# Optimization experiments

Hardware: AMD Instinct MI355X
Metric: run time of the kernel (lower is better)

Reference implementation:

```python
import jax, jax.numpy as jnp
import numpy as np

NEG_SLOPE = 0.2
EPS = 1e-16  # matches PyG softmax epsilon


def gat_conv(x, src, dst, W, att_src, att_dst, bias):
    """PyG-style GATConv (concat heads, self-loops already in src/dst).
    x: [N, F_in]; W: [F_in, H*C]; att_*: [H, C]; bias: [H*C]."""
    N = x.shape[0]
    H, C = att_src.shape
    h = (x @ W).reshape(N, H, C)                       # [N,H,C]
    a_src = jnp.einsum('nhc,hc->nh', h, att_src)       # [N,H]
    a_dst = jnp.einsum('nhc,hc->nh', h, att_dst)
    e = jax.nn.leaky_relu(a_src[src] + a_dst[dst], NEG_SLOPE)   # [E,H]
    # segment softmax over incoming edges of each dst node
    e_max = jax.ops.segment_max(e, dst, num_segments=N)         # [N,H]
    e_max = jnp.where(jnp.isfinite(e_max), e_max, 0.0)
    e_exp = jnp.exp(e - e_max[dst])                              # [E,H]
    denom = jax.ops.segment_sum(e_exp, dst, num_segments=N)     # [N,H]
    alpha = e_exp / (denom[dst] + EPS)                           # [E,H]
    msg = h[src] * alpha[:, :, None]                             # [E,H,C]
    out = jax.ops.segment_sum(msg, dst, num_segments=N)         # [N,H,C]
    return out.reshape(N, H * C) + bias


def setup_inputs() -> dict:
    key = jax.random.key(0)
    ks = jax.random.split(key, 16)
    N, E = 50000, 800000
    F_in, C, H = 1280, 32, 8
    HC = H * C
    NG = 64  # graphs in batch
    x = jax.random.normal(ks[0], (N, F_in), dtype=jnp.float32)
    edge_index = jax.random.randint(ks[1], (2, E), 0, N, dtype=jnp.int64)
    batch = jnp.sort(jax.random.randint(ks[2], (N,), 0, NG, dtype=jnp.int64))
    s = 1.0 / np.sqrt(F_in)
    W1 = jax.random.normal(ks[3], (F_in, HC), dtype=jnp.float32) * s
    as1 = jax.random.normal(ks[4], (H, C), dtype=jnp.float32) * 0.1
    ad1 = jax.random.normal(ks[5], (H, C), dtype=jnp.float32) * 0.1
    b1 = jnp.zeros((HC,), dtype=jnp.float32)
    s2 = 1.0 / np.sqrt(HC)
    W2 = jax.random.normal(ks[6], (HC, HC), dtype=jnp.float32) * s2
    as2 = jax.random.normal(ks[7], (H, C), dtype=jnp.float32) * 0.1
    ad2 = jax.random.normal(ks[8], (H, C), dtype=jnp.float32) * 0.1
    b2 = jnp.zeros((HC,), dtype=jnp.float32)
    lin1_w = jax.random.normal(ks[9], (HC, 128), dtype=jnp.float32) * s2
    lin1_b = jnp.zeros((128,), dtype=jnp.float32)
    lin2_w = jax.random.normal(ks[10], (128, 1), dtype=jnp.float32) * (1.0 / np.sqrt(128))
    lin2_b = jnp.zeros((1,), dtype=jnp.float32)
    return {"x": x, "edge_index": edge_index, "batch": batch,
            "W1": W1, "as1": as1, "ad1": ad1, "b1": b1,
            "W2": W2, "as2": as2, "ad2": ad2, "b2": b2,
            "lin1_w": lin1_w, "lin1_b": lin1_b, "lin2_w": lin2_w, "lin2_b": lin2_b}


def reference(x, edge_index, batch, W1, as1, ad1, b1, W2, as2, ad2, b2,
              lin1_w, lin1_b, lin2_w, lin2_b):
    N = x.shape[0]
    NG = 64
    loops = jnp.arange(N, dtype=edge_index.dtype)
    src = jnp.concatenate([edge_index[0], loops])  # add self-loops (PyG default)
    dst = jnp.concatenate([edge_index[1], loops])
    h = jax.nn.relu(gat_conv(x, src, dst, W1, as1, ad1, b1))
    h = jax.nn.relu(gat_conv(h, src, dst, W2, as2, ad2, b2))
    # global mean pool over graphs
    sums = jax.ops.segment_sum(h, batch, num_segments=NG)               # [NG,HC]
    cnts = jax.ops.segment_sum(jnp.ones((N, 1), h.dtype), batch, num_segments=NG)
    pooled = sums / jnp.maximum(cnts, 1.0)
    z = jax.nn.relu(pooled @ lin1_w + lin1_b)
    out = z @ lin2_w + lin2_b                                            # [NG,1]
    return out.squeeze(-1)
```

## Files before the change

### kernel.cpp

```cpp
#include <hip/hip_runtime.h>
#include <hip/hip_bf16.h>
#include <math.h>

#define HC 256
#define NH 8
#define NEG_SLOPE 0.2f
#define CHW 64

typedef unsigned short u16;
typedef __attribute__((ext_vector_type(8))) short bf16x8;
typedef __attribute__((ext_vector_type(4))) short bf16x4;
typedef __attribute__((ext_vector_type(4))) float f32x4;

__device__ __forceinline__ u16 f2bf(float f) {
    unsigned int u = __float_as_uint(f);
    u += 0x7FFFu + ((u >> 16) & 1u);
    return (u16)(u >> 16);
}
__device__ __forceinline__ float bf2f(u16 s) {
    return __uint_as_float(((unsigned int)s) << 16);
}
__device__ __forceinline__ f32x4 bf4f(ushort4 v) {
    f32x4 r;
    r[0] = bf2f(v.x); r[1] = bf2f(v.y); r[2] = bf2f(v.z); r[3] = bf2f(v.w);
    return r;
}

__global__ __launch_bounds__(256) void pack_b_split(const float* __restrict__ B, int K,
                                                    u16* __restrict__ Bh,
                                                    u16* __restrict__ Bl) {
    const int g = blockIdx.x * 256 + threadIdx.x;
    const int lane = g & 63;
    const int f = (g >> 6) & 15;
    const int kt = g >> 10;
    const int col = f * 16 + (lane & 15);
    const int k0 = kt * 32 + (lane >> 4) * 8;
    bf16x8 hv, lv;
#pragma unroll
    for (int e = 0; e < 8; e++) {
        const float v = B[(size_t)(k0 + e) * HC + col];
        const u16 h = f2bf(v);
        hv[e] = (short)h;
        lv[e] = (short)f2bf(v - bf2f(h));
    }
    const size_t off = (size_t)g * 8;
    *(bf16x8*)(Bh + off) = hv;
    *(bf16x8*)(Bl + off) = lv;
}

__global__ __launch_bounds__(256) void gemm_fused_split(
    const float* __restrict__ A,
    const u16* __restrict__ Bh, const u16* __restrict__ Bl,
    float* __restrict__ C, int M, int K) {
    __shared__ u16 ldsA[2][2048];
    const int tid = threadIdx.x;
    const int wid = tid >> 6;
    const int lane = tid & 63;
    const int rowblk = blockIdx.x;
    const int KT = K >> 5;

    f32x4 acc[4][4];
#pragma unroll
    for (int i = 0; i < 4; i++)
#pragma unroll
        for (int j = 0; j < 4; j++) acc[i][j] = (f32x4)0.f;

    const int srow = wid * 16 + (lane & 15);
    const int skq = (lane >> 4) * 8;
    const int grow = rowblk * 64 + srow;
    const float* aptr = (grow < M) ? (A + (size_t)grow * K + skq) : nullptr;
    const int wslot = wid * 512 + lane * 8;

    auto cvt_store = [&](int buf, float4 v0, float4 v1) {
        const float vv[8] = {v0.x, v0.y, v0.z, v0.w, v1.x, v1.y, v1.z, v1.w};
        bf16x8 hv;
#pragma unroll
        for (int e = 0; e < 8; e++) hv[e] = (short)f2bf(vv[e]);
        *(bf16x8*)&ldsA[buf][wslot] = hv;
    };

    float4 p0 = make_float4(0.f, 0.f, 0.f, 0.f), p1 = p0;
    if (aptr) {
        p0 = *(const float4*)(aptr);
        p1 = *(const float4*)(aptr + 4);
    }
    cvt_store(0, p0, p1);
    p0 = make_float4(0.f, 0.f, 0.f, 0.f); p1 = p0;
    if (aptr && KT > 1) {
        p0 = *(const float4*)(aptr + 32);
        p1 = *(const float4*)(aptr + 36);
    }
    __syncthreads();

    int cur = 0;
    for (int kt = 0; kt < KT; kt++) {
        const u16* bHp = Bh + ((size_t)kt * 16 + wid * 4) * 512 + lane * 8;
        const u16* bLp = Bl + ((size_t)kt * 16 + wid * 4) * 512 + lane * 8;
        bf16x8 bh[4], bl[4];
#pragma unroll
        for (int j = 0; j < 4; j++) {
            bh[j] = *(const bf16x8*)(bHp + j * 512);
            bl[j] = *(const bf16x8*)(bLp + j * 512);
        }
        const u16* base = &ldsA[cur][lane * 8];
        bf16x8 ah[4];
#pragma unroll
        for (int i = 0; i < 4; i++) ah[i] = *(const bf16x8*)(base + i * 512);

        if (kt + 1 < KT) {
            cvt_store(cur ^ 1, p0, p1);
            p0 = make_float4(0.f, 0.f, 0.f, 0.f); p1 = p0;
            if (aptr && kt + 2 < KT) {
                p0 = *(const float4*)(aptr + (kt + 2) * 32);
                p1 = *(const float4*)(aptr + (kt + 2) * 32 + 4);
            }
        }
#pragma unroll
        for (int i = 0; i < 4; i++)
#pragma unroll
            for (int j = 0; j < 4; j++) {
                acc[i][j] = __builtin_amdgcn_mfma_f32_16x16x32_bf16(ah[i], bh[j], acc[i][j], 0, 0, 0);
                acc[i][j] = __builtin_amdgcn_mfma_f32_16x16x32_bf16(ah[i], bl[j], acc[i][j], 0, 0, 0);
            }
        __syncthreads();
        cur ^= 1;
    }

    const int r0 = rowblk * 64;
    const int colb = wid * 64 + (lane & 15);
#pragma unroll
    for (int i = 0; i < 4; i++) {
#pragma unroll
        for (int r = 0; r < 4; r++) {
            const int row = r0 + i * 16 + (lane >> 4) * 4 + r;
            if (row < M) {
#pragma unroll
                for (int j = 0; j < 4; j++)
                    C[(size_t)row * HC + colb + j * 16] = acc[i][j][r];
            }
        }
    }
}

__global__ __launch_bounds__(256) void attn_coef(const float* __restrict__ h,
                                                 const float* __restrict__ att_s,
                                                 const float* __restrict__ att_d,
                                                 float* __restrict__ a_src,
                                                 float* __restrict__ a_dst,
                                                 u16* __restrict__ h_bf) {
    const int n = blockIdx.x;
    const int tid = threadIdx.x;
    const float hv = h[(size_t)n * HC + tid];
    h_bf[(size_t)n * HC + tid] = f2bf(hv);
    float p = hv * att_s[tid];
    float q = hv * att_d[tid];
#pragma unroll
    for (int m = 16; m >= 1; m >>= 1) {
        p += __shfl_xor(p, m);
        q += __shfl_xor(q, m);
    }
    if ((tid & 31) == 0) {
        a_src[n * NH + (tid >> 5)] = p;
        a_dst[n * NH + (tid >> 5)] = q;
    }
}

__global__ void count_deg(const int* __restrict__ dst, int E, int ET, int* __restrict__ deg) {
    const int e = blockIdx.x * blockDim.x + threadIdx.x;
    if (e >= ET) return;
    const int d = (e < E) ? dst[e] : (e - E);
    atomicAdd(&deg[d], 1);
}

__global__ __launch_bounds__(256) void scan_block(const int* __restrict__ deg,
                                                  int* __restrict__ row_ptr,
                                                  int* __restrict__ partials, int N) {
    __shared__ int sd[256];
    const int tid = threadIdx.x;
    const int base = blockIdx.x * 1024 + tid * 4;
    int v0 = (base + 0 < N) ? deg[base + 0] : 0;
    int v1 = (base + 1 < N) ? deg[base + 1] : 0;
    int v2 = (base + 2 < N) ? deg[base + 2] : 0;
    int v3 = (base + 3 < N) ? deg[base + 3] : 0;
    const int tsum = v0 + v1 + v2 + v3;
    sd[tid] = tsum;
    __syncthreads();
    int run = tsum;
    for (int off = 1; off < 256; off <<= 1) {
        int t = 0;
        if (tid >= off) t = sd[tid - off];
        __syncthreads();
        run += t;
        sd[tid] = run;
        __syncthreads();
    }
    const int excl = run - tsum;
    int s0 = excl + v0, s1 = s0 + v1, s2 = s1 + v2, s3 = s2 + v3;
    if (base + 0 < N) row_ptr[base + 1] = s0;
    if (base + 1 < N) row_ptr[base + 2] = s1;
    if (base + 2 < N) row_ptr[base + 3] = s2;
    if (base + 3 < N) row_ptr[base + 4] = s3;
    if (tid == 255) partials[blockIdx.x] = run;
}

__global__ __launch_bounds__(1024) void scan_partials(int* __restrict__ partials, int nb) {
    __shared__ int sd[1024];
    const int tid = threadIdx.x;
    int v = (tid < nb) ? partials[tid] : 0;
    sd[tid] = v;
    __syncthreads();
    int run = v;
    for (int off = 1; off < 1024; off <<= 1) {
        int t = 0;
        if (tid >= off) t = sd[tid - off];
        __syncthreads();
        run += t;
        sd[tid] = run;
        __syncthreads();
    }
    if (tid < nb) partials[tid] = run - v;
}

__global__ __launch_bounds__(256) void scan_add(int* __restrict__ row_ptr,
                                                const int* __restrict__ partials, int N) {
    const int i = blockIdx.x * 256 + threadIdx.x;
    if (i == 0) row_ptr[0] = 0;
    if (i < N) row_ptr[i + 1] += partials[i >> 10];
}

__global__ void scatter_edges(const int* __restrict__ src_in, const int* __restrict__ dst,
                              int E, int ET, const int* __restrict__ row_ptr,
                              int* __restrict__ cursor, int* __restrict__ esrc) {
    const int e = blockIdx.x * blockDim.x + threadIdx.x;
    if (e >= ET) return;
    const int d = (e < E) ? dst[e] : (e - E);
    const int s = (e < E) ? src_in[e] : (e - E);
    const int pos = atomicAdd(&cursor[d], 1);
    esrc[row_ptr[d] + pos] = s;
}

__global__ __launch_bounds__(256) void gat_aggregate_wave(
    const u16* __restrict__ h_bf, const float* __restrict__ a_src,
    const float* __restrict__ a_dst, const int* __restrict__ row_ptr,
    const int* __restrict__ esrc, const float* __restrict__ bias,
    float* __restrict__ out, int N) {
    __shared__ int   s_src[4][CHW];
    __shared__ float s_ev[4][CHW][NH];

    const int tid = threadIdx.x;
    const int wv = tid >> 6;
    const int lane = tid & 63;
    const int n = blockIdx.x * 4 + wv;
    if (n >= N) return;

    const int beg = row_ptr[n];
    const int deg = row_ptr[n + 1] - beg;
    const int jj = lane >> 3;
    const int hh = lane & 7;
    const int g4 = lane >> 3;

    const float adh = a_dst[n * NH + hh];
    float m_run = -1e30f, d_run = 0.f;
    f32x4 acc = (f32x4)0.f;

    for (int c0 = 0; c0 < deg; c0 += CHW) {
        const int chlen = min(CHW, deg - c0);

        float lmax = -1e30f;
        for (int p = 0; p < chlen; p += 8) {
            const int j = p + jj;
            if (j < chlen) {
                const int s = esrc[beg + c0 + j];
                if (hh == 0) s_src[wv][j] = s;
                float v = a_src[s * NH + hh] + adh;
                v = (v > 0.f) ? v : NEG_SLOPE * v;
                s_ev[wv][j][hh] = v;
                lmax = fmaxf(lmax, v);
            }
        }
        lmax = fmaxf(lmax, __shfl_xor(lmax, 8));
        lmax = fmaxf(lmax, __shfl_xor(lmax, 16));
        lmax = fmaxf(lmax, __shfl_xor(lmax, 32));
        const float mo = m_run;
        const float mn = fmaxf(mo, lmax);
        const float scl = __expf(mo - mn);
        m_run = mn;

        float lsum = 0.f;
        for (int p = 0; p < chlen; p += 8) {
            const int j = p + jj;
            if (j < chlen) {
                const float pv = __expf(s_ev[wv][j][hh] - mn);
                s_ev[wv][j][hh] = pv;
                lsum += pv;
            }
        }
        lsum += __shfl_xor(lsum, 8);
        lsum += __shfl_xor(lsum, 16);
        lsum += __shfl_xor(lsum, 32);
        d_run = d_run * scl + lsum;

        __asm__ volatile("s_waitcnt lgkmcnt(0)" ::: "memory");

        const float scl4 = __shfl(scl, g4);
        f32x4 t0 = (f32x4)0.f, t1 = (f32x4)0.f, t2 = (f32x4)0.f, t3 = (f32x4)0.f;
        int j = 0;
        for (; j + 4 <= chlen; j += 4) {
            const int s0 = s_src[wv][j],     s1 = s_src[wv][j + 1];
            const int s2 = s_src[wv][j + 2], s3 = s_src[wv][j + 3];
            const float p0 = s_ev[wv][j][g4],     p1 = s_ev[wv][j + 1][g4];
            const float p2 = s_ev[wv][j + 2][g4], p3 = s_ev[wv][j + 3][g4];
            const f32x4 h0 = bf4f(*(const ushort4*)&h_bf[(size_t)s0 * HC + lane * 4]);
            const f32x4 h1 = bf4f(*(const ushort4*)&h_bf[(size_t)s1 * HC + lane * 4]);
            const f32x4 h2 = bf4f(*(const ushort4*)&h_bf[(size_t)s2 * HC + lane * 4]);
            const f32x4 h3 = bf4f(*(const ushort4*)&h_bf[(size_t)s3 * HC + lane * 4]);
#pragma unroll
            for (int q = 0; q < 4; q++) {
                t0[q] += p0 * h0[q];
                t1[q] += p1 * h1[q];
                t2[q] += p2 * h2[q];
                t3[q] += p3 * h3[q];
            }
        }
        for (; j < chlen; j++) {
            const int s0 = s_src[wv][j];
            const float p0 = s_ev[wv][j][g4];
            const f32x4 h0 = bf4f(*(const ushort4*)&h_bf[(size_t)s0 * HC + lane * 4]);
#pragma unroll
            for (int q = 0; q < 4; q++) t0[q] += p0 * h0[q];
        }
#pragma unroll
        for (int q = 0; q < 4; q++)
            acc[q] = acc[q] * scl4 + ((t0[q] + t1[q]) + (t2[q] + t3[q]));
    }

    const float invd = 1.f / (__shfl(d_run, g4) + 1e-16f);
    const f32x4 bv = *(const f32x4*)&bias[lane * 4];
    f32x4 o;
#pragma unroll
    for (int q = 0; q < 4; q++) o[q] = fmaxf(acc[q] * invd + bv[q], 0.f);
    *(f32x4*)&out[(size_t)n * HC + lane * 4] = o;
}

__global__ __launch_bounds__(256) void pool_partial(const float* __restrict__ h,
                                                    const int* __restrict__ batch, int N,
                                                    float* __restrict__ sums) {
    __shared__ int bs[64];
    const int tid = threadIdx.x;
    const int base = blockIdx.x * 64;
    const int cnt = min(64, N - base);
    if (tid < 64 && tid < cnt) bs[tid] = batch[base + tid];
    __syncthreads();

    float acc = 0.f;
    int cur = bs[0];
    for (int i = 0; i < cnt; i++) {
        const int g = bs[i];
        if (g != cur) {
            atomicAdd(&sums[(size_t)cur * HC + tid], acc);
            acc = 0.f;
            cur = g;
        }
        acc += h[(size_t)(base + i) * HC + tid];
    }
    atomicAdd(&sums[(size_t)cur * HC + tid], acc);
}

__global__ __launch_bounds__(256) void pool_div(float* __restrict__ sums,
                                                const int* __restrict__ batch, int N) {
    const int g = blockIdx.x;
    const int tid = threadIdx.x;
    int lo = 0, hi = N;
    while (lo < hi) {
        const int mid = (lo + hi) >> 1;
        if (batch[mid] < g) lo = mid + 1; else hi = mid;
    }
    const int start = lo;
    hi = N;
    while (lo < hi) {
        const int mid = (lo + hi) >> 1;
        if (batch[mid] < g + 1) lo = mid + 1; else hi = mid;
    }
    const float inv = 1.f / fmaxf((float)(lo - start), 1.0f);
    sums[(size_t)g * HC + tid] *= inv;
}

__global__ __launch_bounds__(128) void mlp_head(const float* __restrict__ pooled,
                                                const float* __restrict__ w1,
                                                const float* __restrict__ b1,
                                                const float* __restrict__ w2,
                                                const float* __restrict__ b2,
                                                float* __restrict__ out) {
    const int g = blockIdx.x;
    const int tid = threadIdx.x;
    __shared__ float p[HC];
    p[tid] = pooled[g * HC + tid];
    p[tid + 128] = pooled[g * HC + tid + 128];
    __syncthreads();
    float z = b1[tid];
#pragma unroll 8
    for (int k = 0; k < HC; k++) z += p[k] * w1[k * 128 + tid];
    z = fmaxf(z, 0.f);
    float t = z * w2[tid];
#pragma unroll
    for (int m = 32; m >= 1; m >>= 1) t += __shfl_xor(t, m);
    __shared__ float ws2[2];
    if ((tid & 63) == 0) ws2[tid >> 6] = t;
    __syncthreads();
    if (tid == 0) out[g] = ws2[0] + ws2[1] + b2[0];
}

extern "C" void kernel_launch(void* const* d_in, const int* in_sizes, int n_in,
                              void* d_out, int out_size, void* d_ws, size_t ws_size,
                              hipStream_t stream) {
    const float* x      = (const float*)d_in[0];
    const int*   ei     = (const int*)d_in[1];
    const int*   batch  = (const int*)d_in[2];
    const float* W1     = (const float*)d_in[3];
    const float* as1    = (const float*)d_in[4];
    const float* ad1    = (const float*)d_in[5];
    const float* b1     = (const float*)d_in[6];
    const float* W2     = (const float*)d_in[7];
    const float* as2    = (const float*)d_in[8];
    const float* ad2    = (const float*)d_in[9];
    const float* b2     = (const float*)d_in[10];
    const float* lin1w  = (const float*)d_in[11];
    const float* lin1b  = (const float*)d_in[12];
    const float* lin2w  = (const float*)d_in[13];
    const float* lin2b  = (const float*)d_in[14];

    const int N   = in_sizes[2];
    const int E   = in_sizes[1] / 2;
    const int ET  = E + N;
    const int Fin = in_sizes[0] / N;
    const int NG  = 64;

    const int nRB = (N + 63) / 64;
    const int nScanBlk = (N + 1023) / 1024;

    const int* src_arr = ei;
    const int* dst_arr = ei + E;

    char* ws = (char*)d_ws;
    size_t off = 0;
    auto alloc = [&](size_t bytes) {
        void* p = ws + off;
        off += (bytes + 255) & ~(size_t)255;
        return p;
    };
    float* h_gemm  = (float*)alloc((size_t)N * HC * sizeof(float));
    float* h_agg   = (float*)alloc((size_t)N * HC * sizeof(float));
    u16*   h_bf    = (u16*)alloc((size_t)N * HC * sizeof(u16));
    float* a_src   = (float*)alloc((size_t)N * NH * sizeof(float));
    float* a_dst   = (float*)alloc((size_t)N * NH * sizeof(float));
    int*   deg     = (int*)alloc((size_t)N * sizeof(int));
    int*   cursor  = (int*)alloc((size_t)N * sizeof(int));
    int*   row_ptr = (int*)alloc((size_t)(N + 1) * sizeof(int));
    int*   partials= (int*)alloc((size_t)1024 * sizeof(int));
    int*   esrc    = (int*)alloc((size_t)ET * sizeof(int));
    float* pooled  = (float*)alloc((size_t)NG * HC * sizeof(float));
    u16* Bh = (u16*)alloc((size_t)Fin * HC * sizeof(u16));
    u16* Bl = (u16*)alloc((size_t)Fin * HC * sizeof(u16));
    (void)ws_size; (void)n_in; (void)out_size;

    hipMemsetAsync(deg, 0, (size_t)N * sizeof(int), stream);
    hipMemsetAsync(cursor, 0, (size_t)N * sizeof(int), stream);
    {
        const int blocks = (ET + 255) / 256;
        count_deg<<<blocks, 256, 0, stream>>>(dst_arr, E, ET, deg);
        scan_block<<<nScanBlk, 256, 0, stream>>>(deg, row_ptr, partials, N);
        scan_partials<<<1, 1024, 0, stream>>>(partials, nScanBlk);
        scan_add<<<(N + 255) / 256, 256, 0, stream>>>(row_ptr, partials, N);
        scatter_edges<<<blocks, 256, 0, stream>>>(src_arr, dst_arr, E, ET, row_ptr,
                                                  cursor, esrc);
    }

    const int aggBlocks = (N + 3) / 4;

    pack_b_split<<<(Fin / 32) * 4, 256, 0, stream>>>(W1, Fin, Bh, Bl);
    gemm_fused_split<<<nRB, 256, 0, stream>>>(x, Bh, Bl, h_gemm, N, Fin);
    attn_coef<<<N, 256, 0, stream>>>(h_gemm, as1, ad1, a_src, a_dst, h_bf);
    gat_aggregate_wave<<<aggBlocks, 256, 0, stream>>>(h_bf, a_src, a_dst, row_ptr,
                                                      esrc, b1, h_agg, N);

    pack_b_split<<<(HC / 32) * 4, 256, 0, stream>>>(W2, HC, Bh, Bl);
    gemm_fused_split<<<nRB, 256, 0, stream>>>(h_agg, Bh, Bl, h_gemm, N, HC);
    attn_coef<<<N, 256, 0, stream>>>(h_gemm, as2, ad2, a_src, a_dst, h_bf);
    gat_aggregate_wave<<<aggBlocks, 256, 0, stream>>>(h_bf, a_src, a_dst, row_ptr,
                                                      esrc, b2, h_agg, N);

    hipMemsetAsync(pooled, 0, (size_t)NG * HC * sizeof(float), stream);
    pool_partial<<<(N + 63) / 64, 256, 0, stream>>>(h_agg, batch, N, pooled);
    pool_div<<<NG, 256, 0, stream>>>(pooled, batch, N);
    mlp_head<<<NG, 128, 0, stream>>>(pooled, lin1w, lin1b, lin2w, lin2b, (float*)d_out);
}
```

Before: 522.6 us.

## Coalesce A tile loads into padded LDS and double-buffer B fragments

The fused split-bf16 GEMM now loads A with four consecutive threads per row, so each row's 32 floats come from one contiguous segment. They are stored into a row-major LDS tile padded to a stride of 40 to limit bank conflicts. The k-loop is unrolled by two, and B high/low fragments for the next k-tile are prefetched into a second register set while the current tile's MFMAs run. This is meant to cut uncoalesced global traffic for A and hide B load latency. In exchange it uses more registers and assumes an even number of k-tiles: with odd KT the second half would run on uninitialized B fragments.

```diff
diff --git a/kernel.cpp b/kernel.cpp
--- a/kernel.cpp
+++ b/kernel.cpp
@@ -52,7 +52,7 @@
     const float* __restrict__ A,
     const u16* __restrict__ Bh, const u16* __restrict__ Bl,
     float* __restrict__ C, int M, int K) {
-    __shared__ u16 ldsA[2][2048];
+    __shared__ u16 ldsA[2][64 * 40];
     const int tid = threadIdx.x;
     const int wid = tid >> 6;
     const int lane = tid & 63;
@@ -65,56 +65,35 @@
 #pragma unroll
         for (int j = 0; j < 4; j++) acc[i][j] = (f32x4)0.f;
 
-    const int srow = wid * 16 + (lane & 15);
-    const int skq = (lane >> 4) * 8;
+    const int srow = tid >> 2;
+    const int sc0 = (tid & 3) * 8;
     const int grow = rowblk * 64 + srow;
-    const float* aptr = (grow < M) ? (A + (size_t)grow * K + skq) : nullptr;
-    const int wslot = wid * 512 + lane * 8;
-
-    auto cvt_store = [&](int buf, float4 v0, float4 v1) {
+    const float* aptr = (grow < M) ? (A + (size_t)grow * K + sc0) : nullptr;
+    const int woff = srow * 40 + sc0;
+
+    auto stage = [&](int buf, float4 v0, float4 v1) {
         const float vv[8] = {v0.x, v0.y, v0.z, v0.w, v1.x, v1.y, v1.z, v1.w};
         bf16x8 hv;
 #pragma unroll
         for (int e = 0; e < 8; e++) hv[e] = (short)f2bf(vv[e]);
-        *(bf16x8*)&ldsA[buf][wslot] = hv;
+        *(bf16x8*)&ldsA[buf][woff] = hv;
     };
-
-    float4 p0 = make_float4(0.f, 0.f, 0.f, 0.f), p1 = p0;
-    if (aptr) {
-        p0 = *(const float4*)(aptr);
-        p1 = *(const float4*)(aptr + 4);
-    }
-    cvt_store(0, p0, p1);
-    p0 = make_float4(0.f, 0.f, 0.f, 0.f); p1 = p0;
-    if (aptr && KT > 1) {
-        p0 = *(const float4*)(aptr + 32);
-        p1 = *(const float4*)(aptr + 36);
-    }
-    __syncthreads();
-
-    int cur = 0;
-    for (int kt = 0; kt < KT; kt++) {
+    auto readA = [&](int buf, bf16x8* ah) {
+#pragma unroll
+        for (int i = 0; i < 4; i++)
+            ah[i] = *(const bf16x8*)&ldsA[buf][(i * 16 + (lane & 15)) * 40 +
+                                              (lane >> 4) * 8];
+    };
+    auto loadB = [&](int kt, bf16x8* bh, bf16x8* bl) {
         const u16* bHp = Bh + ((size_t)kt * 16 + wid * 4) * 512 + lane * 8;
         const u16* bLp = Bl + ((size_t)kt * 16 + wid * 4) * 512 + lane * 8;
-        bf16x8 bh[4], bl[4];
 #pragma unroll
         for (int j = 0; j < 4; j++) {
             bh[j] = *(const bf16x8*)(bHp + j * 512);
             bl[j] = *(const bf16x8*)(bLp + j * 512);
         }
-        const u16* base = &ldsA[cur][lane * 8];
-        bf16x8 ah[4];
-#pragma unroll
-        for (int i = 0; i < 4; i++) ah[i] = *(const bf16x8*)(base + i * 512);
-
-        if (kt + 1 < KT) {
-            cvt_store(cur ^ 1, p0, p1);
-            p0 = make_float4(0.f, 0.f, 0.f, 0.f); p1 = p0;
-            if (aptr && kt + 2 < KT) {
-                p0 = *(const float4*)(aptr + (kt + 2) * 32);
-                p1 = *(const float4*)(aptr + (kt + 2) * 32 + 4);
-            }
-        }
+    };
+    auto mfma_tile = [&](const bf16x8* ah, const bf16x8* bh, const bf16x8* bl) {
 #pragma unroll
         for (int i = 0; i < 4; i++)
 #pragma unroll
@@ -122,6 +101,50 @@
                 acc[i][j] = __builtin_amdgcn_mfma_f32_16x16x32_bf16(ah[i], bh[j], acc[i][j], 0, 0, 0);
                 acc[i][j] = __builtin_amdgcn_mfma_f32_16x16x32_bf16(ah[i], bl[j], acc[i][j], 0, 0, 0);
             }
+    };
+
+    float4 a0 = make_float4(0.f, 0.f, 0.f, 0.f), a1 = a0;
+    if (aptr) {
+        a0 = *(const float4*)(aptr);
+        a1 = *(const float4*)(aptr + 4);
+    }
+    stage(0, a0, a1);
+    a0 = make_float4(0.f, 0.f, 0.f, 0.f); a1 = a0;
+    if (aptr && KT > 1) {
+        a0 = *(const float4*)(aptr + 32);
+        a1 = *(const float4*)(aptr + 36);
+    }
+    __syncthreads();
+
+    bf16x8 b0h[4], b0l[4], b1h[4], b1l[4];
+    loadB(0, b0h, b0l);
+
+    int cur = 0;
+    for (int kt = 0; kt < KT; kt += 2) {
+        if (kt + 1 < KT) loadB(kt + 1, b1h, b1l);
+        bf16x8 ah[4];
+        readA(cur, ah);
+        stage(cur ^ 1, a0, a1);
+        a0 = make_float4(0.f, 0.f, 0.f, 0.f); a1 = a0;
+        if (aptr && kt + 2 < KT) {
+            a0 = *(const float4*)(aptr + (kt + 2) * 32);
+            a1 = *(const float4*)(aptr + (kt + 2) * 32 + 4);
+        }
+        mfma_tile(ah, b0h, b0l);
+        __syncthreads();
+        cur ^= 1;
+
+        if (kt + 2 < KT) loadB(kt + 2, b0h, b0l);
+        readA(cur, ah);
+        if (kt + 2 < KT) {
+            stage(cur ^ 1, a0, a1);
+            a0 = make_float4(0.f, 0.f, 0.f, 0.f); a1 = a0;
+            if (aptr && kt + 3 < KT) {
+                a0 = *(const float4*)(aptr + (kt + 3) * 32);
+                a1 = *(const float4*)(aptr + (kt + 3) * 32 + 4);
+            }
+        }
+        mfma_tile(ah, b1h, b1l);
         __syncthreads();
         cur ^= 1;
     }
```

After: 514.5 us. Within noise of the previous version (-1.5%).

## Deepen GEMM A-staging to four LDS buffers with register-prefetched B

Applied to the files above, without the earlier changes.

Restructures the split-bf16 GEMM main loop into a four-stage LDS ring for the A tile, processed two k-tiles per barrier, with B fragments double-buffered in registers one k-step ahead. This halves the number of block barriers and lets global loads overlap more MFMA work. The A tile now uses a padded row-major layout (stride 40) to reduce LDS bank conflicts, and launch bounds request four blocks per CU. The costs are more registers and LDS, and the loop assumes KT is a multiple of four, which holds for K of 1280 and 256.

```diff
diff --git a/kernel.cpp b/kernel.cpp
--- a/kernel.cpp
+++ b/kernel.cpp
@@ -25,6 +25,13 @@
     r[0] = bf2f(v.x); r[1] = bf2f(v.y); r[2] = bf2f(v.z); r[3] = bf2f(v.w);
     return r;
 }
+
+#define BAR_LDS()                                                  \
+    do {                                                           \
+        asm volatile("s_waitcnt lgkmcnt(0)" ::: "memory");         \
+        __builtin_amdgcn_s_barrier();                              \
+        __builtin_amdgcn_sched_barrier(0);                         \
+    } while (0)
 
 __global__ __launch_bounds__(256) void pack_b_split(const float* __restrict__ B, int K,
                                                     u16* __restrict__ Bh,
@@ -48,11 +55,11 @@
     *(bf16x8*)(Bl + off) = lv;
 }
 
-__global__ __launch_bounds__(256) void gemm_fused_split(
+__global__ __launch_bounds__(256, 4) void gemm_fused_split(
     const float* __restrict__ A,
     const u16* __restrict__ Bh, const u16* __restrict__ Bl,
     float* __restrict__ C, int M, int K) {
-    __shared__ u16 ldsA[2][2048];
+    __shared__ u16 ldsA[4][64 * 40];
     const int tid = threadIdx.x;
     const int wid = tid >> 6;
     const int lane = tid & 63;
@@ -65,56 +72,43 @@
 #pragma unroll
         for (int j = 0; j < 4; j++) acc[i][j] = (f32x4)0.f;
 
-    const int srow = wid * 16 + (lane & 15);
-    const int skq = (lane >> 4) * 8;
+    const int srow = tid >> 2;
+    const int sc0 = (tid & 3) * 8;
     const int grow = rowblk * 64 + srow;
-    const float* aptr = (grow < M) ? (A + (size_t)grow * K + skq) : nullptr;
-    const int wslot = wid * 512 + lane * 8;
-
-    auto cvt_store = [&](int buf, float4 v0, float4 v1) {
+    const float* aptr = (grow < M) ? (A + (size_t)grow * K + sc0) : nullptr;
+    const int woff = srow * 40 + sc0;
+
+    auto loadA = [&](int kt, float4& v0, float4& v1) {
+        v0 = make_float4(0.f, 0.f, 0.f, 0.f);
+        v1 = v0;
+        if (aptr && kt < KT) {
+            v0 = *(const float4*)(aptr + kt * 32);
+            v1 = *(const float4*)(aptr + kt * 32 + 4);
+        }
+    };
+    auto stage = [&](u16* buf, float4 v0, float4 v1) {
         const float vv[8] = {v0.x, v0.y, v0.z, v0.w, v1.x, v1.y, v1.z, v1.w};
         bf16x8 hv;
 #pragma unroll
         for (int e = 0; e < 8; e++) hv[e] = (short)f2bf(vv[e]);
-        *(bf16x8*)&ldsA[buf][wslot] = hv;
+        *(bf16x8*)&buf[woff] = hv;
     };
-
-    float4 p0 = make_float4(0.f, 0.f, 0.f, 0.f), p1 = p0;
-    if (aptr) {
-        p0 = *(const float4*)(aptr);
-        p1 = *(const float4*)(aptr + 4);
-    }
-    cvt_store(0, p0, p1);
-    p0 = make_float4(0.f, 0.f, 0.f, 0.f); p1 = p0;
-    if (aptr && KT > 1) {
-        p0 = *(const float4*)(aptr + 32);
-        p1 = *(const float4*)(aptr + 36);
-    }
-    __syncthreads();
-
-    int cur = 0;
-    for (int kt = 0; kt < KT; kt++) {
+    auto readA = [&](const u16* buf, bf16x8* ah) {
+#pragma unroll
+        for (int i = 0; i < 4; i++)
+            ah[i] = *(const bf16x8*)&buf[(i * 16 + (lane & 15)) * 40 + (lane >> 4) * 8];
+    };
+    auto loadB = [&](int kt, bf16x8* bh, bf16x8* bl) {
+        if (kt >= KT) return;
         const u16* bHp = Bh + ((size_t)kt * 16 + wid * 4) * 512 + lane * 8;
         const u16* bLp = Bl + ((size_t)kt * 16 + wid * 4) * 512 + lane * 8;
-        bf16x8 bh[4], bl[4];
 #pragma unroll
         for (int j = 0; j < 4; j++) {
             bh[j] = *(const bf16x8*)(bHp + j * 512);
             bl[j] = *(const bf16x8*)(bLp + j * 512);
         }
-        const u16* base = &ldsA[cur][lane * 8];
-        bf16x8 ah[4];
-#pragma unroll
-        for (int i = 0; i < 4; i++) ah[i] = *(const bf16x8*)(base + i * 512);
-
-        if (kt + 1 < KT) {
-            cvt_store(cur ^ 1, p0, p1);
-            p0 = make_float4(0.f, 0.f, 0.f, 0.f); p1 = p0;
-            if (aptr && kt + 2 < KT) {
-                p0 = *(const float4*)(aptr + (kt + 2) * 32);
-                p1 = *(const float4*)(aptr + (kt + 2) * 32 + 4);
-            }
-        }
+    };
+    auto mfma_tile = [&](const bf16x8* ah, const bf16x8* bh, const bf16x8* bl) {
 #pragma unroll
         for (int i = 0; i < 4; i++)
 #pragma unroll
@@ -122,8 +116,48 @@
                 acc[i][j] = __builtin_amdgcn_mfma_f32_16x16x32_bf16(ah[i], bh[j], acc[i][j], 0, 0, 0);
                 acc[i][j] = __builtin_amdgcn_mfma_f32_16x16x32_bf16(ah[i], bl[j], acc[i][j], 0, 0, 0);
             }
-        __syncthreads();
-        cur ^= 1;
+    };
+
+    float4 pAa, pAb, pBa, pBb;
+    loadA(0, pAa, pAb);
+    loadA(1, pBa, pBb);
+    stage(ldsA[0], pAa, pAb);
+    stage(ldsA[1], pBa, pBb);
+    loadA(2, pAa, pAb);
+    loadA(3, pBa, pBb);
+    bf16x8 bhA[4], blA[4], bhB[4], blB[4];
+    loadB(0, bhA, blA);
+    BAR_LDS();
+
+    for (int kt0 = 0; kt0 < KT; kt0 += 4) {
+        const bool notLast = (kt0 + 4 < KT);
+        bf16x8 ah[4];
+
+        loadB(kt0 + 1, bhB, blB);
+        readA(ldsA[0], ah);
+        stage(ldsA[2], pAa, pAb);
+        loadA(kt0 + 4, pAa, pAb);
+        mfma_tile(ah, bhA, blA);
+
+        loadB(kt0 + 2, bhA, blA);
+        readA(ldsA[1], ah);
+        stage(ldsA[3], pBa, pBb);
+        loadA(kt0 + 5, pBa, pBb);
+        mfma_tile(ah, bhB, blB);
+        BAR_LDS();
+
+        loadB(kt0 + 3, bhB, blB);
+        readA(ldsA[2], ah);
+        if (notLast) stage(ldsA[0], pAa, pAb);
+        loadA(kt0 + 6, pAa, pAb);
+        mfma_tile(ah, bhA, blA);
+
+        loadB(kt0 + 4, bhA, blA);
+        readA(ldsA[3], ah);
+        if (notLast) stage(ldsA[1], pBa, pBb);
+        loadA(kt0 + 7, pBa, pBb);
+        mfma_tile(ah, bhB, blB);
+        BAR_LDS();
     }
 
     const int r0 = rowblk * 64;
```

Result: slower. 1.263 ms (+141.6%).
